# Kernel tuning notes

Hardware: AMD Instinct MI355X
Metric: run time of the kernel (lower is better)

Reference implementation:

```python
import jax, jax.numpy as jnp
import numpy as np

B, S, HID, NH, HD = 2, 2048, 768, 12, 64
WINDOW = 128           # ModernBERT local attention window
ROPE_THETA = 10000.0   # local_rope_theta (layer_index=0 -> is_local_attention=True)


def _rotate_half(x):
    x1, x2 = jnp.split(x, 2, axis=-1)
    return jnp.concatenate([-x2, x1], axis=-1)


def setup_inputs() -> dict:
    key = jax.random.key(0)
    k1, k2, k3 = jax.random.split(key, 3)
    hidden_embed = jax.random.normal(k1, (B, S, HID), dtype=jnp.float32)
    Wq = jax.random.normal(k2, (HID, HID), dtype=jnp.float32) * (HID ** -0.5)
    Wo = jax.random.normal(k3, (HID, HID), dtype=jnp.float32) * (HID ** -0.5)
    position_index = jnp.arange(S, dtype=jnp.int32).reshape(1, S)
    # sliding-window additive mask: 0 inside window, -inf outside
    i = jnp.arange(S)
    dist = jnp.abs(i[:, None] - i[None, :])
    local_attention_mask = jnp.where(dist <= WINDOW // 2, 0.0, -jnp.inf).astype(jnp.float32)[None, None]
    global_attention_mask = jnp.zeros((1, 1, S, S), dtype=jnp.float32)
    return {
        "hidden_embed": hidden_embed,
        "Wq": Wq,
        "Wo": Wo,
        "local_attention_mask": local_attention_mask,
        "global_attention_mask": global_attention_mask,
        "position_index": position_index,
    }


def reference(hidden_embed, Wq, Wo, local_attention_mask, global_attention_mask, position_index):
    # q projection; NOTE: source has k = q.view(...), v = q.view(...) -> k and v ARE q
    q = hidden_embed @ Wq.T                                  # [B,S,HID]
    q = q.reshape(B, S, NH, HD).transpose(0, 2, 1, 3)        # [B,NH,S,HD]

    # RoPE
    inv_freq = 1.0 / (ROPE_THETA ** (jnp.arange(0, HD, 2, dtype=jnp.float32) / HD))  # [HD/2]
    pos = position_index.reshape(-1).astype(jnp.float32)     # [S]
    freqs = pos[:, None] * inv_freq[None, :]                 # [S,HD/2]
    emb = jnp.concatenate([freqs, freqs], axis=-1)           # [S,HD]
    cos, sin = jnp.cos(emb), jnp.sin(emb)
    q_rot = q * cos + _rotate_half(q) * sin                  # [B,NH,S,HD]
    k_rot = q_rot                                            # k == q before rope -> same after rope
    v = q                                                    # v == q (no rope on v)

    # masked SDPA (local layer -> local sliding-window mask)
    scale = jnp.asarray(HD, jnp.float32) ** -0.5
    scores = jnp.einsum('bhtd,bhsd->bhts', q_rot, k_rot) * scale + local_attention_mask
    attn = jax.nn.softmax(scores, axis=-1)                   # [B,NH,S,S]
    out = jnp.einsum('bhts,bhsd->bhtd', attn, v)             # [B,NH,S,HD]
    out = out.transpose(0, 2, 1, 3).reshape(B, S, HID)
    return out @ Wo.T
```

## Files before the change

### kernel.cpp

```cpp
#include <hip/hip_runtime.h>
#include <hip/hip_bf16.h>
#include <math.h>
#include <stdint.h>

#define B_    2
#define S_    2048
#define HID_  768
#define NH_   12
#define HD_   64
#define NROWS (B_ * S_)
#define N_HID_ELEM (NROWS * HID_)
#define N_W_ELEM   (HID_ * HID_)

#define KW   224
#define KSTR 232

typedef __bf16 bf16x8 __attribute__((ext_vector_type(8)));
typedef float  floatx4 __attribute__((ext_vector_type(4)));

__global__ void convert_inputs_kernel(const float* __restrict__ src_hidden,
                                      const float* __restrict__ src_w1,
                                      const float* __restrict__ src_w2,
                                      __hip_bfloat16* __restrict__ Hb,
                                      __hip_bfloat16* __restrict__ Wqb,
                                      __hip_bfloat16* __restrict__ Wob)
{
    int i = blockIdx.x * blockDim.x + threadIdx.x;
    const float* src;
    __hip_bfloat16* dst;
    int off;
    const int NH4 = N_HID_ELEM / 4, NW4 = N_W_ELEM / 4;
    if (i < NH4)           { src = src_hidden; dst = Hb;  off = i; }
    else if (i < NH4+NW4)  { src = src_w1;     dst = Wqb; off = i - NH4; }
    else if (i < NH4+2*NW4){ src = src_w2;     dst = Wob; off = i - NH4 - NW4; }
    else return;
    float4 v = reinterpret_cast<const float4*>(src)[off];
    __hip_bfloat16 o[4] = { __float2bfloat16(v.x), __float2bfloat16(v.y),
                            __float2bfloat16(v.z), __float2bfloat16(v.w) };
    *reinterpret_cast<uint64_t*>(dst + 4 * (size_t)off) = *reinterpret_cast<uint64_t*>(o);
}

__device__ __forceinline__ void gload_lds16(const __hip_bfloat16* g, __hip_bfloat16* l)
{
    __builtin_amdgcn_global_load_lds(
        (const __attribute__((address_space(1))) void*)g,
        (__attribute__((address_space(3))) void*)l, 16, 0, 0);
}

template<int ROPE>
__global__ __launch_bounds__(512) void gemm64k2(
    const __hip_bfloat16* __restrict__ A,
    const __hip_bfloat16* __restrict__ W,
    __hip_bfloat16* __restrict__ C,
    __hip_bfloat16* __restrict__ C2,
    float* __restrict__ Cf,
    const int* __restrict__ pos_idx,
    int M, int N, int K)
{
    __shared__ __align__(16) __hip_bfloat16 Ald[2][2][2][64][32];
    __shared__ __align__(16) __hip_bfloat16 Wld[2][2][2][64][32];

    const int tid  = threadIdx.x;
    const int kg   = tid >> 8;
    const int wv4  = (tid >> 6) & 3;
    const int lane = tid & 63;
    const int l16  = lane & 15;
    const int quad = lane >> 4;
    const int m0 = blockIdx.x * 64;
    const int n0 = blockIdx.y * 64;

    const int c   = wv4 * 64 + lane;
    const int sr  = c >> 2;
    const int sc8 = (c & 3) * 8;
    const int kbase = kg * 384;

    const __hip_bfloat16* gA = A + (size_t)(m0 + sr) * K + kbase + sc8;
    const __hip_bfloat16* gW = W + (size_t)(n0 + sr) * K + kbase + sc8;

    floatx4 acc[4] = {};
    const int ra = wv4 * 16 + l16;

    gload_lds16(gA,      &Ald[kg][0][0][wv4 * 16][0]);
    gload_lds16(gA + 32, &Ald[kg][0][1][wv4 * 16][0]);
    gload_lds16(gW,      &Wld[kg][0][0][wv4 * 16][0]);
    gload_lds16(gW + 32, &Wld[kg][0][1][wv4 * 16][0]);

#pragma unroll
    for (int it = 0; it < 6; ++it) {
        const int cur = it & 1;
        __syncthreads();
        if (it + 1 < 6) {
            const int nb = (it + 1) & 1;
            const int ko = (it + 1) * 64;
            gload_lds16(gA + ko,      &Ald[kg][nb][0][wv4 * 16][0]);
            gload_lds16(gA + ko + 32, &Ald[kg][nb][1][wv4 * 16][0]);
            gload_lds16(gW + ko,      &Wld[kg][nb][0][wv4 * 16][0]);
            gload_lds16(gW + ko + 32, &Wld[kg][nb][1][wv4 * 16][0]);
        }
#pragma unroll
        for (int ks = 0; ks < 2; ++ks) {
            bf16x8 a = *reinterpret_cast<const bf16x8*>(&Ald[kg][cur][ks][ra][quad * 8]);
#pragma unroll
            for (int u = 0; u < 4; ++u) {
                bf16x8 w = *reinterpret_cast<const bf16x8*>(
                    &Wld[kg][cur][ks][u * 16 + l16][quad * 8]);
                acc[u] = __builtin_amdgcn_mfma_f32_16x16x32_bf16(a, w, acc[u], 0, 0, 0);
            }
        }
    }

    __syncthreads();
    float* Red = reinterpret_cast<float*>(&Ald[0][0][0][0][0]);
    if (kg == 1) {
#pragma unroll
        for (int u = 0; u < 4; ++u)
#pragma unroll
            for (int r = 0; r < 4; ++r)
                Red[(wv4 * 16 + quad * 4 + r) * 68 + u * 16 + l16] = acc[u][r];
    }
    __syncthreads();
    if (kg == 1) return;
#pragma unroll
    for (int u = 0; u < 4; ++u)
#pragma unroll
        for (int r = 0; r < 4; ++r)
            acc[u][r] += Red[(wv4 * 16 + quad * 4 + r) * 68 + u * 16 + l16];

    if (ROPE) {
#pragma unroll
        for (int r = 0; r < 4; ++r) {
            int m = m0 + wv4 * 16 + quad * 4 + r;
            int s = m & (S_ - 1);
            float pos = (float)pos_idx[s];
#pragma unroll
            for (int u = 0; u < 2; ++u) {
                float f = (float)(u * 16 + l16);
                float inv = exp2f(f * (-0.41524101186092024f));
                float sn, cs;
                sincosf(pos * inv, &sn, &cs);
                float q0 = acc[u][r];
                float q1 = acc[u + 2][r];
                size_t base = (size_t)m * HID_ + n0 + u * 16 + l16;
                C [base]      = __float2bfloat16(q0);
                C [base + 32] = __float2bfloat16(q1);
                C2[base]      = __float2bfloat16(q0 * cs - q1 * sn);
                C2[base + 32] = __float2bfloat16(q1 * cs + q0 * sn);
            }
        }
    } else {
#pragma unroll
        for (int u = 0; u < 4; ++u)
#pragma unroll
            for (int r = 0; r < 4; ++r) {
                int row = m0 + wv4 * 16 + quad * 4 + r;
                int col = n0 + u * 16 + l16;
                Cf[(size_t)row * N + col] = acc[u][r];
            }
    }
}

__global__ __launch_bounds__(256) void attn_kernel(
    const __hip_bfloat16* __restrict__ Q,
    const __hip_bfloat16* __restrict__ Qr,
    __hip_bfloat16* __restrict__ O)
{
    __shared__ __align__(16) __hip_bfloat16 Vt[64][KSTR];
    __shared__ __align__(16) __hip_bfloat16 Pl[64][KSTR];

    const int bh = blockIdx.y;
    const int b  = bh / NH_;
    const int h  = bh % NH_;
    const int i0 = blockIdx.x * 64;
    const int tid = threadIdx.x;

    for (int idx = tid; idx < KW * 8; idx += 256) {
        int w  = idx >> 3;
        int d8 = (idx & 7) * 8;
        int j  = i0 - 64 + w;
        int jc = min(max(j, 0), S_ - 1);
        bf16x8 v = *reinterpret_cast<const bf16x8*>(
            Q + ((size_t)(b * S_ + jc)) * HID_ + h * HD_ + d8);
        const __hip_bfloat16* ve = reinterpret_cast<const __hip_bfloat16*>(&v);
#pragma unroll
        for (int e = 0; e < 8; ++e) Vt[d8 + e][w] = ve[e];
    }
    __syncthreads();

    const int wv   = tid >> 6;
    const int lane = tid & 63;
    const int l16  = lane & 15;
    const int quad = lane >> 4;

    floatx4 sc[10] = {};
    const __hip_bfloat16* qrow =
        Qr + ((size_t)(b * S_ + i0 + wv * 16 + l16)) * HID_ + h * HD_ + quad * 8;
#pragma unroll
    for (int ks = 0; ks < 2; ++ks) {
        bf16x8 a = *reinterpret_cast<const bf16x8*>(qrow + ks * 32);
#pragma unroll
        for (int t = 0; t < 10; ++t) {
            int j = i0 - 64 + (wv + t) * 16 + l16;
            int jc = min(max(j, 0), S_ - 1);
            bf16x8 bfr = *reinterpret_cast<const bf16x8*>(
                Qr + ((size_t)(b * S_ + jc)) * HID_ + h * HD_ + ks * 32 + quad * 8);
            sc[t] = __builtin_amdgcn_mfma_f32_16x16x32_bf16(a, bfr, sc[t], 0, 0, 0);
        }
    }

    const float scale = 0.125f;
    float denom[4];
#pragma unroll
    for (int r = 0; r < 4; ++r) {
        const int R = wv * 16 + quad * 4 + r;
        float xv[10];
        float mx = -3.0e38f;
#pragma unroll
        for (int t = 0; t < 10; ++t) {
            int w = (wv + t) * 16 + l16;
            int j = i0 - 64 + w;
            bool valid = (w >= R) && (w <= R + 128) && (j >= 0) && (j < S_);
            float x = valid ? sc[t][r] * scale : -1.0e30f;
            xv[t] = x;
            mx = fmaxf(mx, x);
        }
#pragma unroll
        for (int msk = 1; msk < 16; msk <<= 1) mx = fmaxf(mx, __shfl_xor(mx, msk, 64));
        float sum = 0.f;
#pragma unroll
        for (int t = 0; t < 10; ++t) {
            float p = __expf(xv[t] - mx);
            sum += p;
            Pl[R][(wv + t) * 16 + l16] = __float2bfloat16(p);
        }
#pragma unroll
        for (int msk = 1; msk < 16; msk <<= 1) sum += __shfl_xor(sum, msk, 64);
        denom[r] = sum;
    }
    __syncthreads();

    floatx4 oacc[4] = {};
#pragma unroll
    for (int c = 0; c < 5; ++c) {
        const int base = wv * 16 + c * 32;
        bf16x8 a = *reinterpret_cast<const bf16x8*>(&Pl[wv * 16 + l16][base + quad * 8]);
#pragma unroll
        for (int u = 0; u < 4; ++u) {
            bf16x8 bfr = *reinterpret_cast<const bf16x8*>(&Vt[u * 16 + l16][base + quad * 8]);
            oacc[u] = __builtin_amdgcn_mfma_f32_16x16x32_bf16(a, bfr, oacc[u], 0, 0, 0);
        }
    }

    __syncthreads();
    float* Of = reinterpret_cast<float*>(&Pl[0][0]);
#pragma unroll
    for (int u = 0; u < 4; ++u)
#pragma unroll
        for (int r = 0; r < 4; ++r)
            Of[(wv * 16 + quad * 4 + r) * 68 + u * 16 + l16] = oacc[u][r] / denom[r];
    __syncthreads();
    {
        int row = tid >> 2;
        int seg = (tid & 3) * 16;
        __hip_bfloat16 ob[16];
#pragma unroll
        for (int e = 0; e < 16; ++e)
            ob[e] = __float2bfloat16(Of[row * 68 + seg + e]);
        __hip_bfloat16* dst = O + ((size_t)(b * S_ + i0 + row)) * HID_ + h * HD_ + seg;
        *reinterpret_cast<bf16x8*>(dst)     = *reinterpret_cast<bf16x8*>(ob);
        *reinterpret_cast<bf16x8*>(dst + 8) = *reinterpret_cast<bf16x8*>(ob + 8);
    }
}

extern "C" void kernel_launch(void* const* d_in, const int* in_sizes, int n_in,
                              void* d_out, int out_size, void* d_ws, size_t ws_size,
                              hipStream_t stream)
{
    int ih = -1, iw1 = -1, iw2 = -1, ip = -1;
    for (int i = 0; i < n_in; ++i) {
        int s = in_sizes[i];
        if      (s == N_HID_ELEM && ih < 0) ih = i;
        else if (s == N_W_ELEM)  { if (iw1 < 0) iw1 = i; else if (iw2 < 0) iw2 = i; }
        else if (s == S_ && ip < 0) ip = i;
    }
    if (ih < 0)  ih = 0;
    if (iw1 < 0) iw1 = 1;
    if (iw2 < 0) iw2 = 2;
    if (ip < 0)  ip = 5;

    const float* hidden = (const float*)d_in[ih];
    const float* w1     = (const float*)d_in[iw1];
    const float* w2     = (const float*)d_in[iw2];
    const int*   pos    = (const int*)d_in[ip];

    __hip_bfloat16* Hb  = (__hip_bfloat16*)d_ws;
    __hip_bfloat16* Wqb = Hb  + N_HID_ELEM;
    __hip_bfloat16* Wob = Wqb + N_W_ELEM;
    __hip_bfloat16* Q   = Wob + N_W_ELEM;
    __hip_bfloat16* Qr  = Q   + N_HID_ELEM;
    __hip_bfloat16* AO  = Hb;

    int conv4 = (N_HID_ELEM + 2 * N_W_ELEM) / 4;
    convert_inputs_kernel<<<(conv4 + 255) / 256, 256, 0, stream>>>(
        hidden, w1, w2, Hb, Wqb, Wob);

    dim3 gblk(NROWS / 64, HID_ / 64);

    gemm64k2<1><<<gblk, 512, 0, stream>>>(Hb, Wqb, Q, Qr, nullptr, pos,
                                          NROWS, HID_, HID_);

    attn_kernel<<<dim3(S_ / 64, B_ * NH_), 256, 0, stream>>>(Q, Qr, AO);

    gemm64k2<0><<<gblk, 512, 0, stream>>>(AO, Wob, nullptr, nullptr, (float*)d_out,
                                          nullptr, NROWS, HID_, HID_);
}
```

Before: 143.1 us.

## Precompute RoPE table, pipeline GEMM loads two stages ahead, restructure V staging

The RoPE sin/cos values are now computed once into a table inside the input-conversion kernel and read by the QKV GEMM epilogue, replacing per-element sincos calls. The GEMM K-loop now prefetches two stages ahead, waits on explicit vmcnt counts and uses raw s_barrier with sched_barrier instead of __syncthreads, so global-to-LDS loads can overlap more of the MFMA work. The attention kernel's V transpose load is changed so each thread loads a whole row instead of striding over chunks. The table adds workspace memory and an extra gather in the epilogue, and the manual waitcnt scheme depends on the exact count of outstanding loads.

```diff
diff --git a/kernel.cpp b/kernel.cpp
--- a/kernel.cpp
+++ b/kernel.cpp
@@ -15,29 +15,44 @@
 #define KW   224
 #define KSTR 232
 
+#define TAB_ELEMS (S_ * 32)
+
 typedef __bf16 bf16x8 __attribute__((ext_vector_type(8)));
 typedef float  floatx4 __attribute__((ext_vector_type(4)));
 
 __global__ void convert_inputs_kernel(const float* __restrict__ src_hidden,
                                       const float* __restrict__ src_w1,
                                       const float* __restrict__ src_w2,
+                                      const int*   __restrict__ pos_idx,
                                       __hip_bfloat16* __restrict__ Hb,
                                       __hip_bfloat16* __restrict__ Wqb,
-                                      __hip_bfloat16* __restrict__ Wob)
+                                      __hip_bfloat16* __restrict__ Wob,
+                                      float2* __restrict__ tab)
 {
     int i = blockIdx.x * blockDim.x + threadIdx.x;
-    const float* src;
-    __hip_bfloat16* dst;
-    int off;
     const int NH4 = N_HID_ELEM / 4, NW4 = N_W_ELEM / 4;
-    if (i < NH4)           { src = src_hidden; dst = Hb;  off = i; }
-    else if (i < NH4+NW4)  { src = src_w1;     dst = Wqb; off = i - NH4; }
-    else if (i < NH4+2*NW4){ src = src_w2;     dst = Wob; off = i - NH4 - NW4; }
-    else return;
-    float4 v = reinterpret_cast<const float4*>(src)[off];
-    __hip_bfloat16 o[4] = { __float2bfloat16(v.x), __float2bfloat16(v.y),
-                            __float2bfloat16(v.z), __float2bfloat16(v.w) };
-    *reinterpret_cast<uint64_t*>(dst + 4 * (size_t)off) = *reinterpret_cast<uint64_t*>(o);
+    const int total4 = NH4 + 2 * NW4;
+    if (i < total4) {
+        const float* src;
+        __hip_bfloat16* dst;
+        int off;
+        if (i < NH4)           { src = src_hidden; dst = Hb;  off = i; }
+        else if (i < NH4+NW4)  { src = src_w1;     dst = Wqb; off = i - NH4; }
+        else                   { src = src_w2;     dst = Wob; off = i - NH4 - NW4; }
+        float4 v = reinterpret_cast<const float4*>(src)[off];
+        __hip_bfloat16 o[4] = { __float2bfloat16(v.x), __float2bfloat16(v.y),
+                                __float2bfloat16(v.z), __float2bfloat16(v.w) };
+        *reinterpret_cast<uint64_t*>(dst + 4 * (size_t)off) = *reinterpret_cast<uint64_t*>(o);
+    } else {
+        int t = i - total4;
+        if (t < TAB_ELEMS) {
+            int s = t >> 5, f = t & 31;
+            float inv = exp2f((float)f * (-0.41524101186092024f));
+            float sn, cs;
+            sincosf((float)pos_idx[s] * inv, &sn, &cs);
+            tab[t] = make_float2(cs, sn);
+        }
+    }
 }
 
 __device__ __forceinline__ void gload_lds16(const __hip_bfloat16* g, __hip_bfloat16* l)
@@ -54,7 +69,7 @@
     __hip_bfloat16* __restrict__ C,
     __hip_bfloat16* __restrict__ C2,
     float* __restrict__ Cf,
-    const int* __restrict__ pos_idx,
+    const float2* __restrict__ tab,
     int M, int N, int K)
 {
     __shared__ __align__(16) __hip_bfloat16 Ald[2][2][2][64][32];
@@ -80,23 +95,24 @@
     floatx4 acc[4] = {};
     const int ra = wv4 * 16 + l16;
 
-    gload_lds16(gA,      &Ald[kg][0][0][wv4 * 16][0]);
-    gload_lds16(gA + 32, &Ald[kg][0][1][wv4 * 16][0]);
-    gload_lds16(gW,      &Wld[kg][0][0][wv4 * 16][0]);
-    gload_lds16(gW + 32, &Wld[kg][0][1][wv4 * 16][0]);
+#define STAGE(itx, buf) do {                                          \
+        const int ko_ = (itx) * 64;                                   \
+        gload_lds16(gA + ko_,      &Ald[kg][buf][0][wv4 * 16][0]);    \
+        gload_lds16(gA + ko_ + 32, &Ald[kg][buf][1][wv4 * 16][0]);    \
+        gload_lds16(gW + ko_,      &Wld[kg][buf][0][wv4 * 16][0]);    \
+        gload_lds16(gW + ko_ + 32, &Wld[kg][buf][1][wv4 * 16][0]);    \
+    } while (0)
+
+    STAGE(0, 0);
+    STAGE(1, 1);
 
 #pragma unroll
     for (int it = 0; it < 6; ++it) {
         const int cur = it & 1;
-        __syncthreads();
-        if (it + 1 < 6) {
-            const int nb = (it + 1) & 1;
-            const int ko = (it + 1) * 64;
-            gload_lds16(gA + ko,      &Ald[kg][nb][0][wv4 * 16][0]);
-            gload_lds16(gA + ko + 32, &Ald[kg][nb][1][wv4 * 16][0]);
-            gload_lds16(gW + ko,      &Wld[kg][nb][0][wv4 * 16][0]);
-            gload_lds16(gW + ko + 32, &Wld[kg][nb][1][wv4 * 16][0]);
-        }
+        if (it == 5) { asm volatile("s_waitcnt vmcnt(0)" ::: "memory"); }
+        else         { asm volatile("s_waitcnt vmcnt(4)" ::: "memory"); }
+        __builtin_amdgcn_s_barrier();
+        __builtin_amdgcn_sched_barrier(0);
 #pragma unroll
         for (int ks = 0; ks < 2; ++ks) {
             bf16x8 a = *reinterpret_cast<const bf16x8*>(&Ald[kg][cur][ks][ra][quad * 8]);
@@ -107,7 +123,11 @@
                 acc[u] = __builtin_amdgcn_mfma_f32_16x16x32_bf16(a, w, acc[u], 0, 0, 0);
             }
         }
-    }
+        __builtin_amdgcn_sched_barrier(0);
+        __builtin_amdgcn_s_barrier();
+        if (it + 2 < 6) STAGE(it + 2, cur);
+    }
+#undef STAGE
 
     __syncthreads();
     float* Red = reinterpret_cast<float*>(&Ald[0][0][0][0][0]);
@@ -131,13 +151,10 @@
         for (int r = 0; r < 4; ++r) {
             int m = m0 + wv4 * 16 + quad * 4 + r;
             int s = m & (S_ - 1);
-            float pos = (float)pos_idx[s];
 #pragma unroll
             for (int u = 0; u < 2; ++u) {
-                float f = (float)(u * 16 + l16);
-                float inv = exp2f(f * (-0.41524101186092024f));
-                float sn, cs;
-                sincosf(pos * inv, &sn, &cs);
+                float2 cssn = tab[s * 32 + u * 16 + l16];
+                float cs = cssn.x, sn = cssn.y;
                 float q0 = acc[u][r];
                 float q1 = acc[u + 2][r];
                 size_t base = (size_t)m * HID_ + n0 + u * 16 + l16;
@@ -173,16 +190,17 @@
     const int i0 = blockIdx.x * 64;
     const int tid = threadIdx.x;
 
-    for (int idx = tid; idx < KW * 8; idx += 256) {
-        int w  = idx >> 3;
-        int d8 = (idx & 7) * 8;
-        int j  = i0 - 64 + w;
+    if (tid < KW) {
+        int j  = i0 - 64 + tid;
         int jc = min(max(j, 0), S_ - 1);
-        bf16x8 v = *reinterpret_cast<const bf16x8*>(
-            Q + ((size_t)(b * S_ + jc)) * HID_ + h * HD_ + d8);
-        const __hip_bfloat16* ve = reinterpret_cast<const __hip_bfloat16*>(&v);
-#pragma unroll
-        for (int e = 0; e < 8; ++e) Vt[d8 + e][w] = ve[e];
+        const __hip_bfloat16* vrow = Q + ((size_t)(b * S_ + jc)) * HID_ + h * HD_;
+#pragma unroll
+        for (int d8i = 0; d8i < 8; ++d8i) {
+            bf16x8 v = *reinterpret_cast<const bf16x8*>(vrow + d8i * 8);
+            const __hip_bfloat16* ve = reinterpret_cast<const __hip_bfloat16*>(&v);
+#pragma unroll
+            for (int e = 0; e < 8; ++e) Vt[d8i * 8 + e][tid] = ve[e];
+        }
     }
     __syncthreads();
 
@@ -297,15 +315,17 @@
     __hip_bfloat16* Wob = Wqb + N_W_ELEM;
     __hip_bfloat16* Q   = Wob + N_W_ELEM;
     __hip_bfloat16* Qr  = Q   + N_HID_ELEM;
+    float2*         Tab = reinterpret_cast<float2*>(Qr + N_HID_ELEM);
     __hip_bfloat16* AO  = Hb;
 
     int conv4 = (N_HID_ELEM + 2 * N_W_ELEM) / 4;
-    convert_inputs_kernel<<<(conv4 + 255) / 256, 256, 0, stream>>>(
-        hidden, w1, w2, Hb, Wqb, Wob);
+    int convtot = conv4 + TAB_ELEMS;
+    convert_inputs_kernel<<<(convtot + 255) / 256, 256, 0, stream>>>(
+        hidden, w1, w2, pos, Hb, Wqb, Wob, Tab);
 
     dim3 gblk(NROWS / 64, HID_ / 64);
 
-    gemm64k2<1><<<gblk, 512, 0, stream>>>(Hb, Wqb, Q, Qr, nullptr, pos,
+    gemm64k2<1><<<gblk, 512, 0, stream>>>(Hb, Wqb, Q, Qr, nullptr, Tab,
                                           NROWS, HID_, HID_);
 
     attn_kernel<<<dim3(S_ / 64, B_ * NH_), 256, 0, stream>>>(Q, Qr, AO);
```

New measurement: 139.5 us. 1.03x faster.
